# Optimization experiments

Hardware: AMD Instinct MI355X
Metric: run time of the kernel (lower is better)

The kernel has to match this reference:

```python
import jax, jax.numpy as jnp
import numpy as np

B, N, KLEN, D = 4, 512, 512, 64
TAU = 4.0


def setup_inputs() -> dict:
    key = jax.random.key(0)
    ks = jax.random.split(key, 7)
    s = 1.0 / np.sqrt(2 * D)
    return {
        "Q": jax.random.normal(ks[0], (B, N, D), jnp.float32),
        "K": jax.random.normal(ks[1], (B, KLEN, D), jnp.float32),
        "V": jax.random.normal(ks[2], (B, KLEN, D), jnp.float32),
        # first Linear: torch weight (D, 2D); stored here as x @ W1 form (2D, D)
        "W1": jax.random.uniform(ks[3], (2 * D, D), jnp.float32, -s, s),
        "b1": jax.random.uniform(ks[4], (D,), jnp.float32, -s, s),
        # second Linear: (D, 1) -> stored as (D,) vector, scalar bias
        "W2": jax.random.uniform(ks[5], (D,), jnp.float32, -1.0 / np.sqrt(D), 1.0 / np.sqrt(D)),
        "b2": jax.random.uniform(ks[6], (), jnp.float32, -1.0 / np.sqrt(D), 1.0 / np.sqrt(D)),
    }


def reference(Q, K, V, W1, b1, W2, b2):
    # torch.stack([Q,K],-1).reshape(b,n,k,2d) interleaves features [q0,k0,q1,...],
    # so  interleaved @ W1 == Q @ W1[0::2] + K @ W1[1::2]  (exact algebraic identity).
    Wq = W1[0::2]  # (D, D): rows facing Q features
    Wk = W1[1::2]  # (D, D): rows facing K features
    hq = jnp.einsum('bnd,de->bne', Q, Wq)            # (B, N, D)
    hk = jnp.einsum('bkd,de->bke', K, Wk)            # (B, K, D)
    h = jax.nn.relu(hq[:, :, None, :] + hk[:, None, :, :] + b1)  # (B, N, K, D)
    res = jnp.einsum('bnkd,d->bnk', h, W2) + b2      # (B, N, K)
    att = jax.nn.softmax(res / TAU, axis=-1)         # softmax over keys
    out = jnp.einsum('bnk,bkd->bnd', att, V)         # (B, N, D)
    return out, att
```

## Files before the change

### kernel.cpp

```cpp
#include <hip/hip_runtime.h>

#define BB 4
#define NN 512
#define KK 512
#define DD 64

__global__ __launch_bounds__(256) void mlpattn_hk(const float* __restrict__ Kp,
                                                  const float* __restrict__ W1,
                                                  float* __restrict__ hk) {
    const int lane = threadIdx.x & 63;
    const int wave = threadIdx.x >> 6;
    const int gw = blockIdx.x * 4 + wave;
    const int r0 = gw * 2;
    const float* x0 = Kp + (size_t)r0 * DD;
    const float* x1 = x0 + DD;
    float acc0 = 0.f, acc1 = 0.f;
#pragma unroll
    for (int d = 0; d < DD; ++d) {
        float w = W1[(2 * d + 1) * DD + lane];
        acc0 = fmaf(x0[d], w, acc0);
        acc1 = fmaf(x1[d], w, acc1);
    }
    hk[(size_t)r0 * DD + lane] = acc0;
    hk[(size_t)(r0 + 1) * DD + lane] = acc1;
}

__global__ __launch_bounds__(256) void mlpattn_main(const float* __restrict__ Q,
                                                    const float* __restrict__ V,
                                                    const float* __restrict__ W1,
                                                    const float* __restrict__ b1,
                                                    const float* __restrict__ W2,
                                                    const float* __restrict__ hk,
                                                    float* __restrict__ out,
                                                    float* __restrict__ att_out) {
    __shared__ float s_hk[128 * 65];
    __shared__ float s_att[4 * 512];
    __shared__ float s_part[8 * 128];
    __shared__ float s_hq[4 * 64];
    __shared__ float s_w2[64];

    const int t = threadIdx.x;
    const int b = blockIdx.x >> 7;
    const int ng = blockIdx.x & 127;

    {
        const int lane = t & 63;
        const int row = t >> 6;
        const float* qrow = Q + ((size_t)b * NN + ng * 4 + row) * DD;
        float acc = 0.f;
#pragma unroll
        for (int d = 0; d < DD; ++d)
            acc = fmaf(qrow[d], W1[2 * d * DD + lane], acc);
        s_hq[row * 64 + lane] = acc + b1[lane];
        if (t < 64) s_w2[t] = W2[t];
    }
    __syncthreads();

    const int k = t & 127;
    const int slot = t >> 7;
    const int d0 = slot * 32;
    float rw[32];
#pragma unroll
    for (int j = 0; j < 32; ++j) rw[j] = s_w2[d0 + j];

    const float4* HK4 = (const float4*)(hk + (size_t)b * KK * DD);

    for (int kc = 0; kc < 4; ++kc) {
#pragma unroll
        for (int m = 0; m < 8; ++m) {
            int idx = m * 256 + t;
            int c = idx & 15;
            int kk = idx >> 4;
            float4 v = HK4[(size_t)(kc * 128 + kk) * 16 + c];
            float* dst = &s_hk[kk * 65 + c * 4];
            dst[0] = v.x; dst[1] = v.y; dst[2] = v.z; dst[3] = v.w;
        }
        __syncthreads();

        float acc0 = 0.f, acc1 = 0.f, acc2 = 0.f, acc3 = 0.f;
#pragma unroll
        for (int j = 0; j < 32; ++j) {
            int d = d0 + j;
            float hkv = s_hk[k * 65 + d];
            float w = rw[j];
            float v0 = fmaxf(s_hq[d] + hkv, 0.f);
            float v1 = fmaxf(s_hq[64 + d] + hkv, 0.f);
            float v2 = fmaxf(s_hq[128 + d] + hkv, 0.f);
            float v3 = fmaxf(s_hq[192 + d] + hkv, 0.f);
            acc0 = fmaf(v0, w, acc0);
            acc1 = fmaf(v1, w, acc1);
            acc2 = fmaf(v2, w, acc2);
            acc3 = fmaf(v3, w, acc3);
        }
        s_part[(slot * 4 + 0) * 128 + k] = acc0;
        s_part[(slot * 4 + 1) * 128 + k] = acc1;
        s_part[(slot * 4 + 2) * 128 + k] = acc2;
        s_part[(slot * 4 + 3) * 128 + k] = acc3;
        __syncthreads();

#pragma unroll
        for (int i = 0; i < 2; ++i) {
            int idx = i * 256 + t;
            int row = idx >> 7;
            int kk = idx & 127;
            s_att[row * 512 + kc * 128 + kk] =
                s_part[row * 128 + kk] + s_part[(4 + row) * 128 + kk];
        }
    }
    __syncthreads();

    {
        const int lane = t & 63;
        const int row = t >> 6;
        float* sr = s_att + row * 512;
        float v[8];
        float mx = -1e30f;
#pragma unroll
        for (int i = 0; i < 8; ++i) { v[i] = sr[lane + 64 * i]; mx = fmaxf(mx, v[i]); }
#pragma unroll
        for (int off = 32; off; off >>= 1) mx = fmaxf(mx, __shfl_xor(mx, off, 64));
        float s = 0.f;
#pragma unroll
        for (int i = 0; i < 8; ++i) { v[i] = __expf((v[i] - mx) * 0.25f); s += v[i]; }
#pragma unroll
        for (int off = 32; off; off >>= 1) s += __shfl_xor(s, off, 64);
        float inv = 1.0f / s;
        float* ga = att_out + ((size_t)b * NN + ng * 4 + row) * KK;
#pragma unroll
        for (int i = 0; i < 8; ++i) {
            float a = v[i] * inv;
            sr[lane + 64 * i] = a;
            ga[lane + 64 * i] = a;
        }
    }
    __syncthreads();

    {
        const int dq = t & 15;
        const int kg = t >> 4;
        const float4* V4 = (const float4*)(V + (size_t)b * KK * DD);
        float4 a0 = {0, 0, 0, 0}, a1 = a0, a2 = a0, a3 = a0;
#pragma unroll
        for (int kk = 0; kk < 32; ++kk) {
            int k2 = kg * 32 + kk;
            float4 vv = V4[(size_t)k2 * 16 + dq];
            float p0 = s_att[k2];
            float p1 = s_att[512 + k2];
            float p2 = s_att[1024 + k2];
            float p3 = s_att[1536 + k2];
            a0.x = fmaf(p0, vv.x, a0.x); a0.y = fmaf(p0, vv.y, a0.y);
            a0.z = fmaf(p0, vv.z, a0.z); a0.w = fmaf(p0, vv.w, a0.w);
            a1.x = fmaf(p1, vv.x, a1.x); a1.y = fmaf(p1, vv.y, a1.y);
            a1.z = fmaf(p1, vv.z, a1.z); a1.w = fmaf(p1, vv.w, a1.w);
            a2.x = fmaf(p2, vv.x, a2.x); a2.y = fmaf(p2, vv.y, a2.y);
            a2.z = fmaf(p2, vv.z, a2.z); a2.w = fmaf(p2, vv.w, a2.w);
            a3.x = fmaf(p3, vv.x, a3.x); a3.y = fmaf(p3, vv.y, a3.y);
            a3.z = fmaf(p3, vv.z, a3.z); a3.w = fmaf(p3, vv.w, a3.w);
        }
        float4* pv4 = (float4*)s_hk;
        pv4[(kg * 4 + 0) * 16 + dq] = a0;
        pv4[(kg * 4 + 1) * 16 + dq] = a1;
        pv4[(kg * 4 + 2) * 16 + dq] = a2;
        pv4[(kg * 4 + 3) * 16 + dq] = a3;
    }
    __syncthreads();
    {
        const int row = t >> 6;
        const int d = t & 63;
        float s = 0.f;
#pragma unroll
        for (int kg = 0; kg < 16; ++kg) s += s_hk[kg * 256 + row * 64 + d];
        out[((size_t)b * NN + ng * 4 + row) * DD + d] = s;
    }
}

extern "C" void kernel_launch(void* const* d_in, const int* in_sizes, int n_in,
                              void* d_out, int out_size, void* d_ws, size_t ws_size,
                              hipStream_t stream) {
    const float* Q  = (const float*)d_in[0];
    const float* K  = (const float*)d_in[1];
    const float* V  = (const float*)d_in[2];
    const float* W1 = (const float*)d_in[3];
    const float* b1 = (const float*)d_in[4];
    const float* W2 = (const float*)d_in[5];

    float* out = (float*)d_out;
    float* att = (float*)d_out + BB * NN * DD;
    float* hk = (float*)d_ws;

    mlpattn_hk<<<256, 256, 0, stream>>>(K, W1, hk);
    mlpattn_main<<<512, 256, 0, stream>>>(Q, V, W1, b1, W2, hk, out, att);
}
```

Before: 89.05 us.

## Register-resident hk per key thread, precompute hq, process 8 query rows per block

```diff
diff --git a/kernel.cpp b/kernel.cpp
--- a/kernel.cpp
+++ b/kernel.cpp
@@ -4,115 +4,97 @@
 #define NN 512
 #define KK 512
 #define DD 64
+#define ROWS 8
 
-__global__ __launch_bounds__(256) void mlpattn_hk(const float* __restrict__ Kp,
-                                                  const float* __restrict__ W1,
-                                                  float* __restrict__ hk) {
+
+__global__ __launch_bounds__(256) void mlpattn_proj(const float* __restrict__ Q,
+                                                    const float* __restrict__ Kp,
+                                                    const float* __restrict__ W1,
+                                                    const float* __restrict__ b1,
+                                                    float* __restrict__ hq_ws,
+                                                    float* __restrict__ hkT_ws) {
     const int lane = threadIdx.x & 63;
     const int wave = threadIdx.x >> 6;
-    const int gw = blockIdx.x * 4 + wave;
-    const int r0 = gw * 2;
-    const float* x0 = Kp + (size_t)r0 * DD;
-    const float* x1 = x0 + DD;
-    float acc0 = 0.f, acc1 = 0.f;
+    const int half = blockIdx.x >> 8;
+    const int blk  = blockIdx.x & 255;
+    const int r0 = (blk * 4 + wave) * 2;
+    if (half == 0) {
+        const float* x0 = Q + (size_t)r0 * DD;
+        const float* x1 = x0 + DD;
+        float acc0 = 0.f, acc1 = 0.f;
 #pragma unroll
-    for (int d = 0; d < DD; ++d) {
-        float w = W1[(2 * d + 1) * DD + lane];
-        acc0 = fmaf(x0[d], w, acc0);
-        acc1 = fmaf(x1[d], w, acc1);
+        for (int d = 0; d < DD; ++d) {
+            float w = W1[(2 * d) * DD + lane];
+            acc0 = fmaf(x0[d], w, acc0);
+            acc1 = fmaf(x1[d], w, acc1);
+        }
+        float bb = b1[lane];
+        hq_ws[(size_t)r0 * DD + lane] = acc0 + bb;
+        hq_ws[(size_t)(r0 + 1) * DD + lane] = acc1 + bb;
+    } else {
+        const float* x0 = Kp + (size_t)r0 * DD;
+        const float* x1 = x0 + DD;
+        float acc0 = 0.f, acc1 = 0.f;
+#pragma unroll
+        for (int d = 0; d < DD; ++d) {
+            float w = W1[(2 * d + 1) * DD + lane];
+            acc0 = fmaf(x0[d], w, acc0);
+            acc1 = fmaf(x1[d], w, acc1);
+        }
+        const int b = r0 >> 9;
+        const int k = r0 & 511;
+        const int j4 = lane >> 2, c = lane & 3;
+        float* dst = hkT_ws + ((size_t)(b * 16 + j4) * KK) * 4 + c;
+        dst[(size_t)k * 4] = acc0;
+        dst[(size_t)(k + 1) * 4] = acc1;
     }
-    hk[(size_t)r0 * DD + lane] = acc0;
-    hk[(size_t)(r0 + 1) * DD + lane] = acc1;
 }
 
-__global__ __launch_bounds__(256) void mlpattn_main(const float* __restrict__ Q,
-                                                    const float* __restrict__ V,
-                                                    const float* __restrict__ W1,
-                                                    const float* __restrict__ b1,
-                                                    const float* __restrict__ W2,
-                                                    const float* __restrict__ hk,
-                                                    float* __restrict__ out,
-                                                    float* __restrict__ att_out) {
-    __shared__ float s_hk[128 * 65];
-    __shared__ float s_att[4 * 512];
-    __shared__ float s_part[8 * 128];
-    __shared__ float s_hq[4 * 64];
-    __shared__ float s_w2[64];
+__global__ __launch_bounds__(512, 2) void mlpattn_main(const float* __restrict__ V,
+                                                       const float* __restrict__ W2,
+                                                       const float* __restrict__ hq_ws,
+                                                       const float* __restrict__ hkT_ws,
+                                                       float* __restrict__ out,
+                                                       float* __restrict__ att_out) {
+    __shared__ float s_att[ROWS * KK];
+    __shared__ float4 s_pv[32 * ROWS * 16];
 
     const int t = threadIdx.x;
-    const int b = blockIdx.x >> 7;
-    const int ng = blockIdx.x & 127;
+    const int b  = blockIdx.x >> 6;
+    const int ng = blockIdx.x & 63;
+    const int row0 = ng * ROWS;
 
+    float hkreg[DD];
     {
-        const int lane = t & 63;
-        const int row = t >> 6;
-        const float* qrow = Q + ((size_t)b * NN + ng * 4 + row) * DD;
-        float acc = 0.f;
+        const float4* hkT4 = (const float4*)hkT_ws + (size_t)b * 16 * KK;
 #pragma unroll
-        for (int d = 0; d < DD; ++d)
-            acc = fmaf(qrow[d], W1[2 * d * DD + lane], acc);
-        s_hq[row * 64 + lane] = acc + b1[lane];
-        if (t < 64) s_w2[t] = W2[t];
+        for (int j4 = 0; j4 < 16; ++j4)
+            *(float4*)&hkreg[j4 * 4] = hkT4[(size_t)j4 * KK + t];
     }
-    __syncthreads();
+    float w2r[DD];
+#pragma unroll
+    for (int j4 = 0; j4 < 16; ++j4)
+        *(float4*)&w2r[j4 * 4] = ((const float4*)W2)[j4];
 
-    const int k = t & 127;
-    const int slot = t >> 7;
-    const int d0 = slot * 32;
-    float rw[32];
+    const float* hqb = hq_ws + ((size_t)b * NN + row0) * DD;
 #pragma unroll
-    for (int j = 0; j < 32; ++j) rw[j] = s_w2[d0 + j];
-
-    const float4* HK4 = (const float4*)(hk + (size_t)b * KK * DD);
-
-    for (int kc = 0; kc < 4; ++kc) {
+    for (int r = 0; r < ROWS; ++r) {
+        float hq[DD];
 #pragma unroll
-        for (int m = 0; m < 8; ++m) {
-            int idx = m * 256 + t;
-            int c = idx & 15;
-            int kk = idx >> 4;
-            float4 v = HK4[(size_t)(kc * 128 + kk) * 16 + c];
-            float* dst = &s_hk[kk * 65 + c * 4];
-            dst[0] = v.x; dst[1] = v.y; dst[2] = v.z; dst[3] = v.w;
-        }
-        __syncthreads();
-
-        float acc0 = 0.f, acc1 = 0.f, acc2 = 0.f, acc3 = 0.f;
+        for (int j4 = 0; j4 < 16; ++j4)
+            *(float4*)&hq[j4 * 4] = ((const float4*)(hqb + r * DD))[j4];
+        float a = 0.f;
 #pragma unroll
-        for (int j = 0; j < 32; ++j) {
-            int d = d0 + j;
-            float hkv = s_hk[k * 65 + d];
-            float w = rw[j];
-            float v0 = fmaxf(s_hq[d] + hkv, 0.f);
-            float v1 = fmaxf(s_hq[64 + d] + hkv, 0.f);
-            float v2 = fmaxf(s_hq[128 + d] + hkv, 0.f);
-            float v3 = fmaxf(s_hq[192 + d] + hkv, 0.f);
-            acc0 = fmaf(v0, w, acc0);
-            acc1 = fmaf(v1, w, acc1);
-            acc2 = fmaf(v2, w, acc2);
-            acc3 = fmaf(v3, w, acc3);
-        }
-        s_part[(slot * 4 + 0) * 128 + k] = acc0;
-        s_part[(slot * 4 + 1) * 128 + k] = acc1;
-        s_part[(slot * 4 + 2) * 128 + k] = acc2;
-        s_part[(slot * 4 + 3) * 128 + k] = acc3;
-        __syncthreads();
-
-#pragma unroll
-        for (int i = 0; i < 2; ++i) {
-            int idx = i * 256 + t;
-            int row = idx >> 7;
-            int kk = idx & 127;
-            s_att[row * 512 + kc * 128 + kk] =
-                s_part[row * 128 + kk] + s_part[(4 + row) * 128 + kk];
-        }
+        for (int j = 0; j < DD; ++j)
+            a = fmaf(fmaxf(hq[j] + hkreg[j], 0.f), w2r[j], a);
+        s_att[r * KK + t] = a;
     }
     __syncthreads();
 
     {
         const int lane = t & 63;
-        const int row = t >> 6;
-        float* sr = s_att + row * 512;
+        const int w = t >> 6;
+        float* sr = s_att + w * KK;
         float v[8];
         float mx = -1e30f;
 #pragma unroll
@@ -125,7 +107,7 @@
 #pragma unroll
         for (int off = 32; off; off >>= 1) s += __shfl_xor(s, off, 64);
         float inv = 1.0f / s;
-        float* ga = att_out + ((size_t)b * NN + ng * 4 + row) * KK;
+        float* ga = att_out + ((size_t)b * NN + row0 + w) * KK;
 #pragma unroll
         for (int i = 0; i < 8; ++i) {
             float a = v[i] * inv;
@@ -138,39 +120,50 @@
     {
         const int dq = t & 15;
         const int kg = t >> 4;
-        const float4* V4 = (const float4*)(V + (size_t)b * KK * DD);
-        float4 a0 = {0, 0, 0, 0}, a1 = a0, a2 = a0, a3 = a0;
+        const float4* V4 = (const float4*)V + (size_t)b * KK * 16;
+        float4 a[ROWS];
 #pragma unroll
-        for (int kk = 0; kk < 32; ++kk) {
-            int k2 = kg * 32 + kk;
-            float4 vv = V4[(size_t)k2 * 16 + dq];
-            float p0 = s_att[k2];
-            float p1 = s_att[512 + k2];
-            float p2 = s_att[1024 + k2];
-            float p3 = s_att[1536 + k2];
-            a0.x = fmaf(p0, vv.x, a0.x); a0.y = fmaf(p0, vv.y, a0.y);
-            a0.z = fmaf(p0, vv.z, a0.z); a0.w = fmaf(p0, vv.w, a0.w);
-            a1.x = fmaf(p1, vv.x, a1.x); a1.y = fmaf(p1, vv.y, a1.y);
-            a1.z = fmaf(p1, vv.z, a1.z); a1.w = fmaf(p1, vv.w, a1.w);
-            a2.x = fmaf(p2, vv.x, a2.x); a2.y = fmaf(p2, vv.y, a2.y);
-            a2.z = fmaf(p2, vv.z, a2.z); a2.w = fmaf(p2, vv.w, a2.w);
-            a3.x = fmaf(p3, vv.x, a3.x); a3.y = fmaf(p3, vv.y, a3.y);
-            a3.z = fmaf(p3, vv.z, a3.z); a3.w = fmaf(p3, vv.w, a3.w);
+        for (int r = 0; r < ROWS; ++r) a[r] = make_float4(0.f, 0.f, 0.f, 0.f);
+#pragma unroll
+        for (int kk = 0; kk < 16; ++kk) {
+            const int k = kg * 16 + kk;
+            float4 vv = V4[(size_t)k * 16 + dq];
+#pragma unroll
+            for (int r = 0; r < ROWS; ++r) {
+                float p = s_att[r * KK + k];
+                a[r].x = fmaf(p, vv.x, a[r].x);
+                a[r].y = fmaf(p, vv.y, a[r].y);
+                a[r].z = fmaf(p, vv.z, a[r].z);
+                a[r].w = fmaf(p, vv.w, a[r].w);
+            }
         }
-        float4* pv4 = (float4*)s_hk;
-        pv4[(kg * 4 + 0) * 16 + dq] = a0;
-        pv4[(kg * 4 + 1) * 16 + dq] = a1;
-        pv4[(kg * 4 + 2) * 16 + dq] = a2;
-        pv4[(kg * 4 + 3) * 16 + dq] = a3;
+#pragma unroll
+        for (int r = 0; r < ROWS; ++r)
+            s_pv[(kg * ROWS + r) * 16 + dq] = a[r];
     }
     __syncthreads();
+
+    float4* s_red = (float4*)s_att;
     {
-        const int row = t >> 6;
-        const int d = t & 63;
-        float s = 0.f;
+        const int o = t & 127;
+        const int g = t >> 7;
+        float4 s = make_float4(0.f, 0.f, 0.f, 0.f);
 #pragma unroll
-        for (int kg = 0; kg < 16; ++kg) s += s_hk[kg * 256 + row * 64 + d];
-        out[((size_t)b * NN + ng * 4 + row) * DD + d] = s;
+        for (int i = 0; i < 8; ++i) {
+            float4 p = s_pv[(g * 8 + i) * 128 + o];
+            s.x += p.x; s.y += p.y; s.z += p.z; s.w += p.w;
+        }
+        s_red[g * 128 + o] = s;
+    }
+    __syncthreads();
+    if (t < 128) {
+        float4 s0 = s_red[t], s1 = s_red[128 + t], s2 = s_red[256 + t], s3 = s_red[384 + t];
+        float4 s = make_float4(s0.x + s1.x + s2.x + s3.x,
+                               s0.y + s1.y + s2.y + s3.y,
+                               s0.z + s1.z + s2.z + s3.z,
+                               s0.w + s1.w + s2.w + s3.w);
+        const int r = t >> 4, dq = t & 15;
+        ((float4*)out)[((size_t)b * NN + row0 + r) * 16 + dq] = s;
     }
 }
 
@@ -186,8 +179,9 @@
 
     float* out = (float*)d_out;
     float* att = (float*)d_out + BB * NN * DD;
-    float* hk = (float*)d_ws;
+    float* hq_ws  = (float*)d_ws;
+    float* hkT_ws = (float*)d_ws + BB * NN * DD;
 
-    mlpattn_hk<<<256, 256, 0, stream>>>(K, W1, hk);
-    mlpattn_main<<<512, 256, 0, stream>>>(Q, V, W1, b1, W2, hk, out, att);
+    mlpattn_proj<<<512, 256, 0, stream>>>(Q, K, W1, b1, hq_ws, hkT_ws);
+    mlpattn_main<<<256, 512, 0, stream>>>(V, W2, hq_ws, hkT_ws, out, att);
 }
```

New measurement: 86.64 us. 2.7% less time.
